# Optimization experiments

Hardware: AMD Instinct MI355X
Metric: run time of the kernel (lower is better)

The kernel has to match this reference:

```python
import jax, jax.numpy as jnp
import numpy as np

EPS = 1e-5

def _bn(x, s, b, m, v):
    # inference-mode BatchNorm2d over channel axis of NCHW
    return (x - m[None, :, None, None]) * jax.lax.rsqrt(v[None, :, None, None] + EPS) \
           * s[None, :, None, None] + b[None, :, None, None]

def _conv3(x, w):
    return jax.lax.conv_general_dilated(x, w, (1, 1), 'SAME',
                                        dimension_numbers=('NCHW', 'OIHW', 'NCHW'))

def _conv1(x, w, b):
    # 1x1 conv as einsum; w: [out_c, in_c]
    return jnp.einsum('oc,bchw->bohw', w, x) + b[None, :, None, None]

def _cca(f, qw, qb, kw, kb, vw, vb, gamma):
    # Criss-cross attention (faithful to source: no diagonal -inf masking, INF() unused there)
    B, C, H, W = f.shape
    q = _conv1(f, qw, qb)   # [B, C/8, H, W]
    k = _conv1(f, kw, kb)   # [B, C/8, H, W]
    v = _conv1(f, vw, vb)   # [B, C,   H, W]
    # energy along column (same w, all h') and row (same h, all w')
    eH = jnp.einsum('bchw,bciw->bhwi', q, k)            # [B,H,W,H]
    eW = jnp.einsum('bchw,bchj->bhwj', q, k)            # [B,H,W,W]
    att = jax.nn.softmax(jnp.concatenate([eH, eW], axis=3), axis=3)  # [B,H,W,H+W]
    aH, aW = att[..., :H], att[..., H:]
    oH = jnp.einsum('bhwi,bciw->bchw', aH, v)
    oW = jnp.einsum('bhwj,bchj->bchw', aW, v)
    return gamma * (oH + oW) + f


def setup_inputs() -> dict:
    key = jax.random.key(0)
    ks = iter(jax.random.split(key, 64))
    B, Cin, H, W = 8, 2048, 64, 64
    Ci, Cq, Co = 256, 32, 512
    rn = lambda s, sc=0.02: jax.random.normal(next(ks), s, jnp.float32) * sc
    ru = lambda s: jax.random.uniform(next(ks), s, jnp.float32)
    return {
        'x': jax.random.normal(next(ks), (B, Cin, H, W), jnp.float32),
        'recurrence': 2,
        'conva_w': rn((Ci, Cin, 3, 3)),
        'bn_a_s': ru((Ci,)), 'bn_a_b': rn((Ci,), 0.1), 'bn_a_m': rn((Ci,), 0.1), 'bn_a_v': ru((Ci,)),
        'q_w': rn((Cq, Ci)), 'q_b': rn((Cq,), 0.1),
        'k_w': rn((Cq, Ci)), 'k_b': rn((Cq,), 0.1),
        'v_w': rn((Ci, Ci)), 'v_b': rn((Ci,), 0.1),
        'cca_gamma': rn((1,), 1.0),
        'convb_w': rn((Ci, Ci, 3, 3)),
        'bn_b_s': ru((Ci,)), 'bn_b_b': rn((Ci,), 0.1), 'bn_b_m': rn((Ci,), 0.1), 'bn_b_v': ru((Ci,)),
        'sq_w': rn((Ci, Ci)), 'sq_b': rn((Ci,), 0.1),
        'bn_g_s': ru((Ci,)), 'bn_g_b': rn((Ci,), 0.1), 'bn_g_m': rn((Ci,), 0.1), 'bn_g_v': ru((Ci,)),
        'fc1_w': rn((Ci // 2, Ci)), 'fc1_b': rn((Ci // 2,), 0.1),
        'fc2_w': rn((Ci, Ci // 2)), 'fc2_b': rn((Ci,), 0.1),
        'bott_w': rn((Co, Cin + 2 * Ci, 3, 3)),
        'bn_t_s': ru((Co,)), 'bn_t_b': rn((Co,), 0.1), 'bn_t_m': rn((Co,), 0.1), 'bn_t_v': ru((Co,)),
    }


def reference(x, recurrence, conva_w, bn_a_s, bn_a_b, bn_a_m, bn_a_v,
              q_w, q_b, k_w, k_b, v_w, v_b, cca_gamma,
              convb_w, bn_b_s, bn_b_b, bn_b_m, bn_b_v,
              sq_w, sq_b, bn_g_s, bn_g_b, bn_g_m, bn_g_v,
              fc1_w, fc1_b, fc2_w, fc2_b,
              bott_w, bn_t_s, bn_t_b, bn_t_m, bn_t_v):
    out = _bn(_conv3(x, conva_w), bn_a_s, bn_a_b, bn_a_m, bn_a_v)
    # Global_Avg_Pooling (SE gating) on conva output
    fm = jax.nn.relu(_bn(_conv1(out, sq_w, sq_b), bn_g_s, bn_g_b, bn_g_m, bn_g_v))
    vec = fm.mean(axis=(-2, -1))                       # [B, Ci]
    h = jax.nn.relu(vec @ fc1_w.T + fc1_b)
    gate = jax.nn.sigmoid(h @ fc2_w.T + fc2_b)
    out_gap = out * gate[:, :, None, None]
    # recurrent criss-cross attention
    for _ in range(recurrence):
        out = _cca(out, q_w, q_b, k_w, k_b, v_w, v_b, cca_gamma)
    out = _bn(_conv3(out, convb_w), bn_b_s, bn_b_b, bn_b_m, bn_b_v)
    cat = jnp.concatenate([x, out, out_gap], axis=1)   # [B, Cin+2*Ci, H, W]
    return _bn(_conv3(cat, bott_w), bn_t_s, bn_t_b, bn_t_m, bn_t_v)
```

## Files before the change

### kernel.cpp

```cpp
#include <hip/hip_runtime.h>
#include <hip/hip_bf16.h>

typedef unsigned short u16;
typedef unsigned int u32;
typedef __attribute__((ext_vector_type(8))) short short8;
typedef __attribute__((ext_vector_type(8))) unsigned short u16x8;
typedef __attribute__((ext_vector_type(4))) unsigned short u16x4;
typedef __attribute__((ext_vector_type(4))) float f32x4;

#define BN_EPS 1e-5f
#define PADW 66
#define CATC 2560

__device__ __forceinline__ u16 f2b(float f) {
    __hip_bfloat16 h = __float2bfloat16(f);
    return *reinterpret_cast<u16*>(&h);
}
__device__ __forceinline__ float b2f(u16 u) {
    __hip_bfloat16 h;
    *reinterpret_cast<u16*>(&h) = u;
    return __bfloat162float(h);
}
__device__ __forceinline__ void async_copy16(void* lds, const void* g) {
    __builtin_amdgcn_global_load_lds((const __attribute__((address_space(1))) u32*)g,
                                     (__attribute__((address_space(3))) u32*)lds, 16, 0, 0);
}
__device__ __forceinline__ void fence_() { asm volatile("" ::: "memory"); }
__device__ __forceinline__ void barrier_() { fence_(); __builtin_amdgcn_s_barrier(); fence_(); }

template<int TAPS, int BN, int EPI, int CPT, int NTILES, int KSPLIT>
__global__ __launch_bounds__(512, 2)
void gemm8(const u16* __restrict__ Ag, int cstride,
           const u16* __restrict__ Bg, int ktot_full, int klen,
           const float* __restrict__ alpha, const float* __restrict__ beta,
           u16* __restrict__ outb, int ostride, int ochoff,
           float* __restrict__ outf, int nch)
{
    constexpr int WN   = BN / 4;
    constexpr int NSUB = WN / 16;
    constexpr int NQ   = NSUB / 2;
    constexpr int BLH  = BN / 128;
    constexpr int ASZ  = 256 * 128;
    constexpr int BSZ  = BN * 128;
    const int KT = klen / 64;

    extern __shared__ __align__(16) char smem[];
    char* smA = smem;
    char* smB = smem + 2 * ASZ;

    const int tid  = threadIdx.x;
    const int lane = tid & 63;
    const int wave = tid >> 6;
    const int wr = wave >> 2;
    const int wc = wave & 3;

    const int nwg = gridDim.x;
    const int wg  = blockIdx.x;
    const int swz = (wg & 7) * (nwg >> 3) + (wg >> 3);
    const int sel = swz % (NTILES * KSPLIT);
    const int m0  = (swz / (NTILES * KSPLIT)) * 256;
    const int n0  = (sel / KSPLIT) * BN;
    const int ks  = sel % KSPLIT;
    const int kstart = ks * klen;

    const int sr = tid >> 3;
    const int sc = tid & 7;
    const int scx8 = (sc ^ (sr & 7)) * 8;
    long baseAe[4];
#pragma unroll
    for (int j = 0; j < 4; ++j) {
        int p = m0 + j * 64 + sr;
        int b = p >> 12, h = (p >> 6) & 63, w = p & 63;
        long apix = (TAPS == 1) ? ((long)(b * PADW + h + 1) * PADW + (w + 1))
                                : ((long)(b * PADW + h) * PADW + w);
        baseAe[j] = apix * cstride + scx8;
    }
    long baseBe[2 * BLH];
#pragma unroll
    for (int h = 0; h < 2; ++h)
#pragma unroll
        for (int l = 0; l < BLH; ++l)
            baseBe[h * BLH + l] = (long)(n0 + h * (BN / 2) + l * 64 + sr) * ktot_full + scx8;

    auto stA = [&](int bsel, int h, long aoff) {
#pragma unroll
        for (int l = 0; l < 2; ++l) {
            const u16* g = Ag + baseAe[2 * h + l] + aoff;
            async_copy16(smA + bsel * ASZ + h * 16384 + l * 8192 + tid * 16, g);
        }
    };
    auto stB = [&](int bsel, int h, int k0) {
#pragma unroll
        for (int l = 0; l < BLH; ++l) {
            const u16* g = Bg + baseBe[h * BLH + l] + k0;
            async_copy16(smB + bsel * BSZ + h * (BSZ / 2) + l * 8192 + tid * 16, g);
        }
    };

    const int rsel  = lane & 15;
    const int cswz0 = (((lane >> 4)     ^ (lane & 7)) << 4);
    const int cswz1 = (((4 | (lane >> 4)) ^ (lane & 7)) << 4);

    f32x4 acc[8][NSUB] = {};
    short8 a0f[4][2], a1f[4][2], b0[NQ][2], b1[NQ][2];

    auto ldA = [&](int bsel, int mh, short8 (&aa)[4][2]) {
        const char* base = smA + bsel * ASZ + (wr * 128 + mh * 64 + rsel) * 128;
#pragma unroll
        for (int mi = 0; mi < 4; ++mi) {
            aa[mi][0] = *(const short8*)(base + mi * 2048 + cswz0);
            aa[mi][1] = *(const short8*)(base + mi * 2048 + cswz1);
        }
    };
    auto ldB = [&](int bsel, int nh, short8 (&bb)[NQ][2]) {
        const char* base = smB + bsel * BSZ + (wc * WN + nh * (WN / 2) + rsel) * 128;
#pragma unroll
        for (int nj = 0; nj < NQ; ++nj) {
            bb[nj][0] = *(const short8*)(base + nj * 2048 + cswz0);
            bb[nj][1] = *(const short8*)(base + nj * 2048 + cswz1);
        }
    };
    auto quad = [&](int MH, int NH, short8 (&aa)[4][2], short8 (&bb)[NQ][2]) {
#pragma unroll
        for (int mi = 0; mi < 4; ++mi)
#pragma unroll
            for (int nj = 0; nj < NQ; ++nj)
#pragma unroll
                for (int kk = 0; kk < 2; ++kk)
                    acc[MH * 4 + mi][NH * NQ + nj] =
                        __builtin_amdgcn_mfma_f32_16x16x32_bf16(
                            aa[mi][kk], bb[nj][kk], acc[MH * 4 + mi][NH * NQ + nj], 0, 0, 0);
    };

    const int tap0 = kstart / CPT;
    int c0_ = kstart - tap0 * CPT;
    int dx_ = tap0 % 3;
    long aoff_ = ((long)dx_ + (long)(tap0 / 3) * PADW) * cstride + c0_;
    auto adv = [&]() {
        c0_ += 64; aoff_ += 64;
        if (c0_ == CPT) {
            c0_ = 0; aoff_ += (long)cstride - CPT;
            if (++dx_ == 3) { dx_ = 0; aoff_ += (long)(PADW - 3) * cstride; }
        }
    };

    stA(0, 0, aoff_); stA(0, 1, aoff_); stB(0, 0, kstart); stB(0, 1, kstart);
    adv();
    stA(1, 0, aoff_); stA(1, 1, aoff_); stB(1, 0, kstart + 64); stB(1, 1, kstart + 64);
    int skb = kstart + 128;

    asm volatile("s_waitcnt vmcnt(8)" ::: "memory");
    barrier_();

    for (int kt = 0; kt < KT; ++kt) {
        const int buf = kt & 1;
        ldA(buf, 0, a0f); ldB(buf, 0, b0); ldB(buf, 1, b1); ldA(buf, 1, a1f);
        if (kt >= 1 && kt + 1 < KT) { stA(buf ^ 1, 0, aoff_); stA(buf ^ 1, 1, aoff_); }
        __builtin_amdgcn_s_setprio(1);
        quad(0, 0, a0f, b0);
        quad(0, 1, a0f, b1);
        __builtin_amdgcn_s_setprio(0);
        barrier_();
        if (kt + 2 < KT) { stB(buf, 0, skb); stB(buf, 1, skb); }
        __builtin_amdgcn_s_setprio(1);
        quad(1, 0, a1f, b0);
        quad(1, 1, a1f, b1);
        __builtin_amdgcn_s_setprio(0);
        if (kt + 2 < KT) {
            asm volatile("s_waitcnt vmcnt(4)" ::: "memory");
        } else {
            asm volatile("s_waitcnt vmcnt(0)" ::: "memory");
        }
        barrier_();
        adv(); skb += 64;
    }

    const int nl = lane & 15, mq = lane >> 4;
#pragma unroll
    for (int s = 0; s < 8; ++s) {
#pragma unroll
        for (int nj = 0; nj < NSUB; ++nj) {
            int n = n0 + wc * WN + nj * 16 + nl;
            float al = (EPI == 4) ? 1.f : alpha[n];
            float be = (EPI == 4) ? 0.f : beta[n];
#pragma unroll
            for (int r = 0; r < 4; ++r) {
                int m = m0 + wr * 128 + s * 16 + mq * 4 + r;
                float v = acc[s][nj][r] * al + be;
                if (EPI == 0) {
                    int b = m >> 12, h = (m >> 6) & 63, w = m & 63;
                    long addr = ((long)(b * PADW + h + 1) * PADW + (w + 1)) * ostride + ochoff + n;
                    outb[addr] = f2b(v);
                } else if (EPI == 2) {
                    int b = m >> 12, h = (m >> 6) & 63, w = m & 63;
                    outf[((long)(b * nch + n) << 12) + (h * 64 + w)] = v;
                } else {
                    outf[(long)ks * ((long)32768 * nch) + (long)m * nch + n] = v;
                }
            }
        }
    }
}

__global__ void combine_k(const float* __restrict__ P,
                          const float* __restrict__ alpha, const float* __restrict__ beta,
                          u16* __restrict__ dst, int dstride, int choff)
{
    int t = threadIdx.x;
    int m = blockIdx.x * 4 + (t >> 6);
    int n = (t & 63) * 4;
    int b = m >> 12, h = (m >> 6) & 63, w = m & 63;
    f32x4 v0 = *(const f32x4*)&P[(long)m * 256 + n];
    f32x4 v1 = *(const f32x4*)&P[(long)32768 * 256 + (long)m * 256 + n];
    f32x4 al = *(const f32x4*)&alpha[n];
    f32x4 be = *(const f32x4*)&beta[n];
    u16x4 r;
#pragma unroll
    for (int i = 0; i < 4; ++i) r[i] = f2b((v0[i] + v1[i]) * al[i] + be[i]);
    *(u16x4*)&dst[((long)(b * PADW + h + 1) * PADW + (w + 1)) * dstride + choff + n] = r;
}

__global__ void border_k(u16* __restrict__ cat, u16* __restrict__ f0)
{
    int i = blockIdx.x;
    int b = i / 260, r = i - b * 260;
    int ph, pw;
    if (r < 66)       { ph = 0;        pw = r; }
    else if (r < 132) { ph = 65;       pw = r - 66; }
    else if (r < 196) { ph = r - 131;  pw = 0; }
    else              { ph = r - 195;  pw = 65; }
    long pix = (long)(b * PADW + ph) * PADW + pw;
    int t = threadIdx.x;
    u16x8 z = {};
    *(u16x8*)&cat[pix * CATC + t * 8] = z;
    if (t < 64) *(u16x8*)&cat[pix * CATC + 2048 + t * 8] = z;
    if (t < 32) *(u16x8*)&f0[pix * 256 + t * 8] = z;
}

template<int TAPS, int EPI>
__global__ __launch_bounds__(256, 2)
void gemm_conv(const u16* __restrict__ A, int cstride, int cpt,
               const u16* __restrict__ Bw, int ktot,
               const float* __restrict__ alpha, const float* __restrict__ beta,
               u16* __restrict__ outb, int ostride, int ochoff,
               float* __restrict__ outf, int n_total)
{
    __shared__ u16 As[128][32];
    __shared__ u16 Bs[128][32];
    __shared__ float red[128];

    const int tid  = threadIdx.x;
    const int lane = tid & 63;
    const int wave = tid >> 6;
    const int wr = wave >> 1, wc = wave & 1;
    const int m0 = blockIdx.y * 128;
    const int n0 = blockIdx.x * 128;

    long pixbase[2];
    long browk[2];
#pragma unroll
    for (int i = 0; i < 2; ++i) {
        int row = i * 64 + (tid >> 2);
        int p = m0 + row;
        int b = p >> 12, h = (p >> 6) & 63, w = p & 63;
        if (TAPS == 1) pixbase[i] = (long)(b * PADW + h + 1) * PADW + (w + 1);
        else           pixbase[i] = (long)(b * PADW + h) * PADW + w;
        browk[i] = (long)(n0 + row) * ktot;
    }
    const int chunk = (tid & 3) * 8;

    f32x4 acc[4][4] = {};

    const int steps = ktot / 32;
    int c0 = 0, dx = 0;
    long toff = 0;
    for (int s = 0; s < steps; ++s) {
        const int k0 = s * 32;
#pragma unroll
        for (int i = 0; i < 2; ++i) {
            const u16* ga = A + (pixbase[i] + ((TAPS == 1) ? 0 : toff)) * cstride + c0 + chunk;
            async_copy16((char*)(&As[0][0]) + i * 4096 + tid * 16, ga);
            const u16* gb = Bw + browk[i] + k0 + chunk;
            async_copy16((char*)(&Bs[0][0]) + i * 4096 + tid * 16, gb);
        }
        asm volatile("s_waitcnt vmcnt(0)" ::: "memory");
        __syncthreads();

        short8 af[4], bf[4];
#pragma unroll
        for (int x = 0; x < 4; ++x) {
            af[x] = *(const short8*)&As[wr * 64 + x * 16 + (lane & 15)][(lane >> 4) * 8];
            bf[x] = *(const short8*)&Bs[wc * 64 + x * 16 + (lane & 15)][(lane >> 4) * 8];
        }
#pragma unroll
        for (int mi = 0; mi < 4; ++mi)
#pragma unroll
            for (int ni = 0; ni < 4; ++ni)
                acc[mi][ni] = __builtin_amdgcn_mfma_f32_16x16x32_bf16(af[mi], bf[ni], acc[mi][ni], 0, 0, 0);
        __syncthreads();

        c0 += 32;
        if (TAPS > 1 && c0 == cpt) {
            c0 = 0; dx++; toff += 1;
            if (dx == 3) { dx = 0; toff += PADW - 3; }
        }
    }

    const int nl = lane & 15;
    const int mq = lane >> 4;

    if (EPI == 3) {
        if (tid < 128) red[tid] = 0.f;
        __syncthreads();
#pragma unroll
        for (int ni = 0; ni < 4; ++ni) {
            int ncol = wc * 64 + ni * 16 + nl;
            int n = n0 + ncol;
            float aa = alpha[n], bb = beta[n];
            float ssum = 0.f;
#pragma unroll
            for (int mi = 0; mi < 4; ++mi)
#pragma unroll
                for (int r = 0; r < 4; ++r)
                    ssum += fmaxf(acc[mi][ni][r] * aa + bb, 0.f);
            atomicAdd(&red[ncol], ssum);
        }
        __syncthreads();
        if (tid < 128) {
            int b = m0 >> 12;
            atomicAdd(&outf[b * 256 + n0 + tid], red[tid]);
        }
    } else {
#pragma unroll
        for (int mi = 0; mi < 4; ++mi) {
#pragma unroll
            for (int r = 0; r < 4; ++r) {
                int m = m0 + wr * 64 + mi * 16 + mq * 4 + r;
#pragma unroll
                for (int ni = 0; ni < 4; ++ni) {
                    int n = n0 + wc * 64 + ni * 16 + nl;
                    float v = acc[mi][ni][r] * alpha[n] + beta[n];
                    outb[(long)m * ostride + n] = f2b(v);
                }
            }
        }
    }
}

__global__ void xpad_k(const float* __restrict__ x, u16* __restrict__ cat)
{
    __shared__ float T[64][68];
    int bh = blockIdx.y;
    int b = bh >> 6, h = bh & 63;
    int c0 = blockIdx.x * 64;
    int t = threadIdx.x;
    const float* xb = x + (((long)b * 2048 + c0) * 64 + h) * 64;
#pragma unroll
    for (int i = 0; i < 4; ++i) {
        int idx = i * 256 + t;
        int c = idx >> 4, wq = (idx & 15) * 4;
        *(f32x4*)&T[c][wq] = *(const f32x4*)&xb[(long)c * 4096 + wq];
    }
    __syncthreads();
    long pbase = ((long)(b * PADW + h + 1) * PADW + 1) * CATC + c0;
#pragma unroll
    for (int j = 0; j < 2; ++j) {
        int idx = j * 256 + t;
        int w = idx >> 3, cg = (idx & 7) * 8;
        u16x8 r;
#pragma unroll
        for (int u = 0; u < 8; ++u) r[u] = f2b(T[cg + u][w]);
        *(u16x8*)&cat[pbase + (long)w * CATC + cg] = r;
    }
}

__global__ void prep_w3(const float* __restrict__ w, u16* __restrict__ o, int O, int C)
{
    int idx = blockIdx.x * 256 + threadIdx.x;
    if (idx >= O * C) return;
    int oo = idx / C, c = idx - oo * C;
    const float* s = w + (long)idx * 9;
    long base = (long)oo * 9 * C + c;
#pragma unroll
    for (int t = 0; t < 9; ++t) o[base + (long)t * C] = f2b(s[t]);
}

__global__ void prep_qkv(const float* __restrict__ qw, const float* __restrict__ kw,
                         const float* __restrict__ vw, u16* __restrict__ o)
{
    int idx = blockIdx.x * 256 + threadIdx.x;
    int n = idx >> 8, c = idx & 255;
    float v;
    if (n < 32) v = qw[n * 256 + c];
    else if (n < 64) v = kw[(n - 32) * 256 + c];
    else if (n < 320) v = vw[(n - 64) * 256 + c];
    else v = 0.f;
    o[idx] = f2b(v);
}

__global__ void prep_cast(const float* __restrict__ w, u16* __restrict__ o, int n)
{
    int i = blockIdx.x * 256 + threadIdx.x;
    if (i < n) o[i] = f2b(w[i]);
}

__global__ void prep_ab(const float* as, const float* ab, const float* am, const float* av,
                        const float* gs, const float* gb, const float* gm, const float* gv, const float* sqb,
                        const float* bs, const float* bb, const float* bm, const float* bv,
                        const float* ts, const float* tb, const float* tm, const float* tv,
                        const float* qb, const float* kb, const float* vb,
                        float* Aa, float* Ba_, float* Ag, float* Bg, float* Ab2, float* Bb2,
                        float* At, float* Bt, float* Aq, float* Bq)
{
    int i = blockIdx.x * 256 + threadIdx.x;
    if (i < 256) { float al = as[i] * rsqrtf(av[i] + BN_EPS); Aa[i] = al; Ba_[i] = ab[i] - am[i] * al; }
    else if (i < 512) { int n = i - 256; float al = gs[n] * rsqrtf(gv[n] + BN_EPS); Ag[n] = al; Bg[n] = gb[n] - gm[n] * al + sqb[n] * al; }
    else if (i < 768) { int n = i - 512; float al = bs[n] * rsqrtf(bv[n] + BN_EPS); Ab2[n] = al; Bb2[n] = bb[n] - bm[n] * al; }
    else if (i < 1280) { int n = i - 768; float al = ts[n] * rsqrtf(tv[n] + BN_EPS); At[n] = al; Bt[n] = tb[n] - tm[n] * al; }
    else if (i < 1664) { int n = i - 1280; Aq[n] = 1.f; Bq[n] = (n < 32) ? qb[n] : (n < 64) ? kb[n - 32] : (n < 320) ? vb[n - 64] : 0.f; }
}

__global__ void gate_k(const float* __restrict__ vacc, const float* __restrict__ fc1w,
                       const float* __restrict__ fc1b, const float* __restrict__ fc2w,
                       const float* __restrict__ fc2b, float* __restrict__ gate)
{
    __shared__ float v[256], hbuf[128];
    int b = blockIdx.x, t = threadIdx.x;
    v[t] = vacc[b * 256 + t] * (1.f / 4096.f);
    __syncthreads();
    if (t < 128) {
        float s = fc1b[t];
        for (int c = 0; c < 256; ++c) s += v[c] * fc1w[t * 256 + c];
        hbuf[t] = fmaxf(s, 0.f);
    }
    __syncthreads();
    float s = fc2b[t];
    for (int j = 0; j < 128; ++j) s += hbuf[j] * fc2w[t * 128 + j];
    gate[b * 256 + t] = 1.f / (1.f + __expf(-s));
}

__global__ void gap_k(const u16* __restrict__ f0, const float* __restrict__ gate, u16* __restrict__ cat)
{
    int p = blockIdx.x, t = threadIdx.x;
    int b = p >> 12, h = (p >> 6) & 63, w = p & 63;
    long ppad = (long)(b * PADW + h + 1) * PADW + (w + 1);
    float f = b2f(f0[ppad * 256 + t]);
    cat[ppad * CATC + 2304 + t] = f2b(f * gate[b * 256 + t]);
}

__global__ void gram_k(const u16* __restrict__ qkv, float* eH, float* eW)
{
    __shared__ u16 Qs[64][32];
    __shared__ u16 Ks[64][32];
    int g = blockIdx.x;
    int mode = g >> 9;
    int bx = g & 511;
    int b = bx >> 6, s = bx & 63;
    float* e = mode ? eW : eH;
    int tid = threadIdx.x, lane = tid & 63, wave = tid >> 6;
    {
        int r = tid >> 2, ch = (tid & 3) * 8;
        long pix = (mode == 0) ? ((long)(b * 64 + r) * 64 + s) : ((long)(b * 64 + s) * 64 + r);
        const u16* gp = qkv + pix * 384;
        *(u16x8*)&Qs[r][ch] = *(const u16x8*)(gp + ch);
        *(u16x8*)&Ks[r][ch] = *(const u16x8*)(gp + 32 + ch);
    }
    __syncthreads();
    f32x4 acc[4] = {};
    short8 a = *(const short8*)&Qs[wave * 16 + (lane & 15)][(lane >> 4) * 8];
#pragma unroll
    for (int ni = 0; ni < 4; ++ni) {
        short8 bb = *(const short8*)&Ks[ni * 16 + (lane & 15)][(lane >> 4) * 8];
        acc[ni] = __builtin_amdgcn_mfma_f32_16x16x32_bf16(a, bb, acc[ni], 0, 0, 0);
    }
#pragma unroll
    for (int ni = 0; ni < 4; ++ni)
#pragma unroll
        for (int r = 0; r < 4; ++r) {
            int row = wave * 16 + (lane >> 4) * 4 + r;
            int col = ni * 16 + (lane & 15);
            long pix = (mode == 0) ? ((long)(b * 64 + row) * 64 + s) : ((long)(b * 64 + s) * 64 + row);
            e[pix * 64 + col] = acc[ni][r];
        }
}

__global__ void softmax_k(const float* __restrict__ eH, const float* __restrict__ eW,
                          u16* __restrict__ aH, u16* __restrict__ aW)
{
    long row = blockIdx.x * 4 + (threadIdx.x >> 6);
    int lane = threadIdx.x & 63;
    float v0 = eH[row * 64 + lane];
    float v1 = eW[row * 64 + lane];
    float m = fmaxf(v0, v1);
#pragma unroll
    for (int off = 32; off; off >>= 1) m = fmaxf(m, __shfl_xor(m, off));
    float e0 = __expf(v0 - m), e1 = __expf(v1 - m);
    float s = e0 + e1;
#pragma unroll
    for (int off = 32; off; off >>= 1) s += __shfl_xor(s, off);
    float inv = 1.f / s;
    aH[row * 64 + lane] = f2b(e0 * inv);
    aW[row * 64 + lane] = f2b(e1 * inv);
}

__global__ __launch_bounds__(256, 2)
void oh_k(const u16* __restrict__ aH, const u16* __restrict__ qkv, float* __restrict__ oHb)
{
    __shared__ float Al[64][68];
    __shared__ u16 Vl[64][264];
    int bx = blockIdx.x;
    int b = bx >> 6, w = bx & 63;
    int t = threadIdx.x;
#pragma unroll
    for (int pass = 0; pass < 2; ++pass) {
        int r = pass * 32 + (t >> 3);
        int ch = (t & 7) * 8;
        u16x8 v = *(const u16x8*)(aH + ((long)(b * 64 + r) * 64 + w) * 64 + ch);
        f32x4 s0, s1;
#pragma unroll
        for (int u = 0; u < 4; ++u) { s0[u] = b2f(v[u]); s1[u] = b2f(v[4 + u]); }
        *(f32x4*)&Al[r][ch] = s0;
        *(f32x4*)&Al[r][ch + 4] = s1;
    }
#pragma unroll
    for (int pass = 0; pass < 8; ++pass) {
        int i = pass * 8 + (t >> 5);
        int ch = (t & 31) * 8;
        *(u16x8*)&Vl[i][ch] = *(const u16x8*)(qkv + ((long)(b * 64 + i) * 64 + w) * 384 + 64 + ch);
    }
    __syncthreads();
    int hb = (t >> 5) * 8, cb = (t & 31) * 8;
    float acc[8][8] = {};
    for (int i = 0; i < 64; ++i) {
        float av[8], vv[8];
        u16x8 v8 = *(const u16x8*)&Vl[i][cb];
#pragma unroll
        for (int u = 0; u < 8; ++u) av[u] = Al[hb + u][i];
#pragma unroll
        for (int u = 0; u < 8; ++u) vv[u] = b2f(v8[u]);
#pragma unroll
        for (int u = 0; u < 8; ++u)
#pragma unroll
            for (int x = 0; x < 8; ++x)
                acc[u][x] += av[u] * vv[x];
    }
#pragma unroll
    for (int u = 0; u < 8; ++u) {
        long base = ((long)(b * 64 + hb + u) * 64 + w) * 256 + cb;
        f32x4 s0, s1;
#pragma unroll
        for (int x = 0; x < 4; ++x) { s0[x] = acc[u][x]; s1[x] = acc[u][4 + x]; }
        *(f32x4*)&oHb[base] = s0;
        *(f32x4*)&oHb[base + 4] = s1;
    }
}

__global__ __launch_bounds__(256, 2)
void ow_k(const u16* __restrict__ aW, const u16* __restrict__ qkv, const float* __restrict__ oHb,
          const u16* __restrict__ fin, u16* __restrict__ fout, const float* __restrict__ gamma_p)
{
    __shared__ float Al[64][68];
    __shared__ u16 Vl[64][264];
    int bx = blockIdx.x;
    int b = bx >> 6, h = bx & 63;
    int t = threadIdx.x;
    float gamma = gamma_p[0];
#pragma unroll
    for (int pass = 0; pass < 2; ++pass) {
        int r = pass * 32 + (t >> 3);
        int ch = (t & 7) * 8;
        u16x8 v = *(const u16x8*)(aW + ((long)(b * 64 + h) * 64 + r) * 64 + ch);
        f32x4 s0, s1;
#pragma unroll
        for (int u = 0; u < 4; ++u) { s0[u] = b2f(v[u]); s1[u] = b2f(v[4 + u]); }
        *(f32x4*)&Al[r][ch] = s0;
        *(f32x4*)&Al[r][ch + 4] = s1;
    }
#pragma unroll
    for (int pass = 0; pass < 8; ++pass) {
        int j = pass * 8 + (t >> 5);
        int ch = (t & 31) * 8;
        *(u16x8*)&Vl[j][ch] = *(const u16x8*)(qkv + ((long)(b * 64 + h) * 64 + j) * 384 + 64 + ch);
    }
    __syncthreads();
    int wb = (t >> 5) * 8, cb = (t & 31) * 8;
    float acc[8][8] = {};
    for (int j = 0; j < 64; ++j) {
        float av[8], vv[8];
        u16x8 v8 = *(const u16x8*)&Vl[j][cb];
#pragma unroll
        for (int u = 0; u < 8; ++u) av[u] = Al[wb + u][j];
#pragma unroll
        for (int u = 0; u < 8; ++u) vv[u] = b2f(v8[u]);
#pragma unroll
        for (int u = 0; u < 8; ++u)
#pragma unroll
            for (int x = 0; x < 8; ++x)
                acc[u][x] += av[u] * vv[x];
    }
#pragma unroll
    for (int u = 0; u < 8; ++u) {
        int w = wb + u;
        long pix = ((long)(b * 64 + h) * 64 + w) * 256 + cb;
        long pp = ((long)(b * PADW + h + 1) * PADW + (w + 1)) * 256 + cb;
        u16x8 f8 = *(const u16x8*)&fin[pp];
        f32x4 o0 = *(const f32x4*)&oHb[pix];
        f32x4 o1 = *(const f32x4*)&oHb[pix + 4];
        u16x8 r8;
#pragma unroll
        for (int x = 0; x < 8; ++x) {
            float o = acc[u][x] + ((x < 4) ? o0[x] : o1[x - 4]);
            r8[x] = f2b(gamma * o + b2f(f8[x]));
        }
        *(u16x8*)&fout[pp] = r8;
    }
}

extern "C" void kernel_launch(void* const* d_in, const int* in_sizes, int n_in,
                              void* d_out, int out_size, void* d_ws, size_t ws_size,
                              hipStream_t stream)
{
    const float* x       = (const float*)d_in[0];
    const float* conva_w = (const float*)d_in[2];
    const float* bn_a_s  = (const float*)d_in[3];
    const float* bn_a_b  = (const float*)d_in[4];
    const float* bn_a_m  = (const float*)d_in[5];
    const float* bn_a_v  = (const float*)d_in[6];
    const float* q_w     = (const float*)d_in[7];
    const float* q_b     = (const float*)d_in[8];
    const float* k_w     = (const float*)d_in[9];
    const float* k_b     = (const float*)d_in[10];
    const float* v_w     = (const float*)d_in[11];
    const float* v_b     = (const float*)d_in[12];
    const float* gamma   = (const float*)d_in[13];
    const float* convb_w = (const float*)d_in[14];
    const float* bn_b_s  = (const float*)d_in[15];
    const float* bn_b_b  = (const float*)d_in[16];
    const float* bn_b_m  = (const float*)d_in[17];
    const float* bn_b_v  = (const float*)d_in[18];
    const float* sq_w    = (const float*)d_in[19];
    const float* sq_b    = (const float*)d_in[20];
    const float* bn_g_s  = (const float*)d_in[21];
    const float* bn_g_b  = (const float*)d_in[22];
    const float* bn_g_m  = (const float*)d_in[23];
    const float* bn_g_v  = (const float*)d_in[24];
    const float* fc1_w   = (const float*)d_in[25];
    const float* fc1_b   = (const float*)d_in[26];
    const float* fc2_w   = (const float*)d_in[27];
    const float* fc2_b   = (const float*)d_in[28];
    const float* bott_w  = (const float*)d_in[29];
    const float* bn_t_s  = (const float*)d_in[30];
    const float* bn_t_b  = (const float*)d_in[31];
    const float* bn_t_m  = (const float*)d_in[32];
    const float* bn_t_v  = (const float*)d_in[33];

    char* ws = (char*)d_ws;
    size_t off = 0;
    auto alloc = [&](size_t bytes) { char* p = ws + off; off += (bytes + 255) & ~(size_t)255; return p; };

    u16*   CAT  = (u16*)  alloc((size_t)8 * PADW * PADW * CATC * 2);
    u16*   F0   = (u16*)  alloc((size_t)8 * PADW * PADW * 256 * 2);
    u16*   F1   = (u16*)  alloc((size_t)8 * PADW * PADW * 256 * 2);
    size_t cca_off = off;
    u16*   QKV  = (u16*)  alloc((size_t)32768 * 384 * 2);
    float* EH   = (float*)alloc((size_t)32768 * 64 * 4);
    float* EWb  = (float*)alloc((size_t)32768 * 64 * 4);
    u16*   AH   = (u16*)  alloc((size_t)32768 * 64 * 2);
    u16*   AW   = (u16*)  alloc((size_t)32768 * 64 * 2);
    float* OHB  = (float*)alloc((size_t)32768 * 256 * 4);
    float* P    = (float*)(ws + cca_off);
    u16*   WA   = (u16*)  alloc((size_t)256 * 18432 * 2);
    u16*   WB   = (u16*)  alloc((size_t)256 * 2304 * 2);
    u16*   WT   = (u16*)  alloc((size_t)512 * 23040 * 2);
    u16*   WQKV = (u16*)  alloc((size_t)384 * 256 * 2);
    u16*   WSQ  = (u16*)  alloc((size_t)256 * 256 * 2);
    float* Aa   = (float*)alloc(256 * 4);
    float* Ba_  = (float*)alloc(256 * 4);
    float* Ag   = (float*)alloc(256 * 4);
    float* Bg   = (float*)alloc(256 * 4);
    float* Ab2  = (float*)alloc(256 * 4);
    float* Bb2  = (float*)alloc(256 * 4);
    float* At   = (float*)alloc(512 * 4);
    float* Bt   = (float*)alloc(512 * 4);
    float* Aq   = (float*)alloc(384 * 4);
    float* Bq   = (float*)alloc(384 * 4);
    float* VACC = (float*)alloc(8 * 256 * 4);
    float* GATE = (float*)alloc(8 * 256 * 4);

    hipFuncSetAttribute((const void*)gemm8<9, 256, 4, 2048, 1, 2>,
                        hipFuncAttributeMaxDynamicSharedMemorySize, 131072);
    hipFuncSetAttribute((const void*)gemm8<9, 256, 4, 256, 1, 2>,
                        hipFuncAttributeMaxDynamicSharedMemorySize, 131072);
    hipFuncSetAttribute((const void*)gemm8<9, 256, 2, 2560, 2, 1>,
                        hipFuncAttributeMaxDynamicSharedMemorySize, 131072);

    hipMemsetAsync(VACC, 0, 8 * 256 * 4, stream);

    border_k<<<8 * 260, 256, 0, stream>>>(CAT, F0);
    prep_w3<<<(256 * 2048 + 255) / 256, 256, 0, stream>>>(conva_w, WA, 256, 2048);
    prep_w3<<<(256 * 256 + 255) / 256, 256, 0, stream>>>(convb_w, WB, 256, 256);
    prep_w3<<<(512 * 2560 + 255) / 256, 256, 0, stream>>>(bott_w, WT, 512, 2560);
    prep_qkv<<<384, 256, 0, stream>>>(q_w, k_w, v_w, WQKV);
    prep_cast<<<256, 256, 0, stream>>>(sq_w, WSQ, 65536);
    prep_ab<<<7, 256, 0, stream>>>(bn_a_s, bn_a_b, bn_a_m, bn_a_v,
                                   bn_g_s, bn_g_b, bn_g_m, bn_g_v, sq_b,
                                   bn_b_s, bn_b_b, bn_b_m, bn_b_v,
                                   bn_t_s, bn_t_b, bn_t_m, bn_t_v,
                                   q_b, k_b, v_b,
                                   Aa, Ba_, Ag, Bg, Ab2, Bb2, At, Bt, Aq, Bq);
    xpad_k<<<dim3(32, 512), 256, 0, stream>>>(x, CAT);

    gemm8<9, 256, 4, 2048, 1, 2><<<256, 512, 131072, stream>>>(
        CAT, CATC, WA, 18432, 9216, Aa, Ba_, nullptr, 0, 0, P, 256);
    combine_k<<<8192, 256, 0, stream>>>(P, Aa, Ba_, F0, 256, 0);

    gemm_conv<1, 3><<<dim3(2, 256), 256, 0, stream>>>(F0, 256, 256, WSQ, 256, Ag, Bg, nullptr, 0, 0, VACC, 0);
    gate_k<<<8, 256, 0, stream>>>(VACC, fc1_w, fc1_b, fc2_w, fc2_b, GATE);
    gap_k<<<32768, 256, 0, stream>>>(F0, GATE, CAT);

    for (int rec = 0; rec < 2; ++rec) {
        u16* fin = rec ? F1 : F0;
        u16* fout = rec ? F0 : F1;
        gemm_conv<1, 1><<<dim3(3, 256), 256, 0, stream>>>(fin, 256, 256, WQKV, 256, Aq, Bq, QKV, 384, 0, nullptr, 0);
        gram_k<<<1024, 256, 0, stream>>>(QKV, EH, EWb);
        softmax_k<<<8192, 256, 0, stream>>>(EH, EWb, AH, AW);
        oh_k<<<512, 256, 0, stream>>>(AH, QKV, OHB);
        ow_k<<<512, 256, 0, stream>>>(AW, QKV, OHB, fin, fout, gamma);
    }

    gemm8<9, 256, 4, 256, 1, 2><<<256, 512, 131072, stream>>>(
        F0, 256, WB, 2304, 1152, Ab2, Bb2, nullptr, 0, 0, P, 256);
    combine_k<<<8192, 256, 0, stream>>>(P, Ab2, Bb2, CAT, CATC, 2048);

    gemm8<9, 256, 2, 2560, 2, 1><<<256, 512, 131072, stream>>>(
        CAT, CATC, WT, 23040, 23040, At, Bt, nullptr, 0, 0, (float*)d_out, 512);
}
```

Baseline: 1.173 ms.

## Load GEMM weight fragments directly from global memory instead of staging in LDS

The conv-GEMM kernel stops staging the weight (B) tile through shared memory. Each wave now reads its B fragments straight from global memory into registers each k-step, and LDS use is halved to A only. The pipeline is reduced to a single barrier per iteration with a full vmcnt(0) wait. This trims LDS traffic and footprint, but the B loads become uncoalesced per-wave global reads that sit on the critical path with no prefetch. The two-phase overlap of the old loop is also lost.

```diff
diff --git a/kernel.cpp b/kernel.cpp
--- a/kernel.cpp
+++ b/kernel.cpp
@@ -39,14 +39,11 @@
     constexpr int WN   = BN / 4;
     constexpr int NSUB = WN / 16;
     constexpr int NQ   = NSUB / 2;
-    constexpr int BLH  = BN / 128;
     constexpr int ASZ  = 256 * 128;
-    constexpr int BSZ  = BN * 128;
     const int KT = klen / 64;
 
     extern __shared__ __align__(16) char smem[];
     char* smA = smem;
-    char* smB = smem + 2 * ASZ;
 
     const int tid  = threadIdx.x;
     const int lane = tid & 63;
@@ -75,12 +72,6 @@
                                 : ((long)(b * PADW + h) * PADW + w);
         baseAe[j] = apix * cstride + scx8;
     }
-    long baseBe[2 * BLH];
-#pragma unroll
-    for (int h = 0; h < 2; ++h)
-#pragma unroll
-        for (int l = 0; l < BLH; ++l)
-            baseBe[h * BLH + l] = (long)(n0 + h * (BN / 2) + l * 64 + sr) * ktot_full + scx8;
 
     auto stA = [&](int bsel, int h, long aoff) {
 #pragma unroll
@@ -89,20 +80,15 @@
             async_copy16(smA + bsel * ASZ + h * 16384 + l * 8192 + tid * 16, g);
         }
     };
-    auto stB = [&](int bsel, int h, int k0) {
-#pragma unroll
-        for (int l = 0; l < BLH; ++l) {
-            const u16* g = Bg + baseBe[h * BLH + l] + k0;
-            async_copy16(smB + bsel * BSZ + h * (BSZ / 2) + l * 8192 + tid * 16, g);
-        }
-    };
 
     const int rsel  = lane & 15;
     const int cswz0 = (((lane >> 4)     ^ (lane & 7)) << 4);
     const int cswz1 = (((4 | (lane >> 4)) ^ (lane & 7)) << 4);
 
+    const u16* Bbase = Bg + (long)(n0 + wc * 64 + rsel) * ktot_full + ((lane >> 4) * 8);
+
     f32x4 acc[8][NSUB] = {};
-    short8 a0f[4][2], a1f[4][2], b0[NQ][2], b1[NQ][2];
+    short8 a0f[4][2], a1f[4][2], bb0[NQ][2], bb1[NQ][2];
 
     auto ldA = [&](int bsel, int mh, short8 (&aa)[4][2]) {
         const char* base = smA + bsel * ASZ + (wr * 128 + mh * 64 + rsel) * 128;
@@ -112,13 +98,13 @@
             aa[mi][1] = *(const short8*)(base + mi * 2048 + cswz1);
         }
     };
-    auto ldB = [&](int bsel, int nh, short8 (&bb)[NQ][2]) {
-        const char* base = smB + bsel * BSZ + (wc * WN + nh * (WN / 2) + rsel) * 128;
-#pragma unroll
-        for (int nj = 0; nj < NQ; ++nj) {
-            bb[nj][0] = *(const short8*)(base + nj * 2048 + cswz0);
-            bb[nj][1] = *(const short8*)(base + nj * 2048 + cswz1);
-        }
+    auto ldBg = [&](int nh, int k0, short8 (&bb)[NQ][2]) {
+#pragma unroll
+        for (int nj = 0; nj < NQ; ++nj)
+#pragma unroll
+            for (int kk = 0; kk < 2; ++kk)
+                bb[nj][kk] = *(const short8*)(Bbase + (long)(nh * 32 + nj * 16) * ktot_full
+                                              + k0 + kk * 32);
     };
     auto quad = [&](int MH, int NH, short8 (&aa)[4][2], short8 (&bb)[NQ][2]) {
 #pragma unroll
@@ -144,35 +130,28 @@
         }
     };
 
-    stA(0, 0, aoff_); stA(0, 1, aoff_); stB(0, 0, kstart); stB(0, 1, kstart);
+    stA(0, 0, aoff_); stA(0, 1, aoff_);
     adv();
-    stA(1, 0, aoff_); stA(1, 1, aoff_); stB(1, 0, kstart + 64); stB(1, 1, kstart + 64);
-    int skb = kstart + 128;
-
-    asm volatile("s_waitcnt vmcnt(8)" ::: "memory");
+    stA(1, 0, aoff_); stA(1, 1, aoff_);
+
+    asm volatile("s_waitcnt vmcnt(4)" ::: "memory");
     barrier_();
 
+    int kB = kstart;
     for (int kt = 0; kt < KT; ++kt) {
         const int buf = kt & 1;
-        ldA(buf, 0, a0f); ldB(buf, 0, b0); ldB(buf, 1, b1); ldA(buf, 1, a1f);
+        ldBg(0, kB, bb0); ldBg(1, kB, bb1);
+        ldA(buf, 0, a0f); ldA(buf, 1, a1f);
         if (kt >= 1 && kt + 1 < KT) { stA(buf ^ 1, 0, aoff_); stA(buf ^ 1, 1, aoff_); }
         __builtin_amdgcn_s_setprio(1);
-        quad(0, 0, a0f, b0);
-        quad(0, 1, a0f, b1);
+        quad(0, 0, a0f, bb0);
+        quad(0, 1, a0f, bb1);
+        quad(1, 0, a1f, bb0);
+        quad(1, 1, a1f, bb1);
         __builtin_amdgcn_s_setprio(0);
+        asm volatile("s_waitcnt vmcnt(0)" ::: "memory");
         barrier_();
-        if (kt + 2 < KT) { stB(buf, 0, skb); stB(buf, 1, skb); }
-        __builtin_amdgcn_s_setprio(1);
-        quad(1, 0, a1f, b0);
-        quad(1, 1, a1f, b1);
-        __builtin_amdgcn_s_setprio(0);
-        if (kt + 2 < KT) {
-            asm volatile("s_waitcnt vmcnt(4)" ::: "memory");
-        } else {
-            asm volatile("s_waitcnt vmcnt(0)" ::: "memory");
-        }
-        barrier_();
-        adv(); skb += 64;
+        adv(); kB += 64;
     }
 
     const int nl = lane & 15, mq = lane >> 4;
@@ -688,11 +667,11 @@
     float* GATE = (float*)alloc(8 * 256 * 4);
 
     hipFuncSetAttribute((const void*)gemm8<9, 256, 4, 2048, 1, 2>,
-                        hipFuncAttributeMaxDynamicSharedMemorySize, 131072);
+                        hipFuncAttributeMaxDynamicSharedMemorySize, 65536);
     hipFuncSetAttribute((const void*)gemm8<9, 256, 4, 256, 1, 2>,
-                        hipFuncAttributeMaxDynamicSharedMemorySize, 131072);
+                        hipFuncAttributeMaxDynamicSharedMemorySize, 65536);
     hipFuncSetAttribute((const void*)gemm8<9, 256, 2, 2560, 2, 1>,
-                        hipFuncAttributeMaxDynamicSharedMemorySize, 131072);
+                        hipFuncAttributeMaxDynamicSharedMemorySize, 65536);
 
     hipMemsetAsync(VACC, 0, 8 * 256 * 4, stream);
 
@@ -710,7 +689,7 @@
                                    Aa, Ba_, Ag, Bg, Ab2, Bb2, At, Bt, Aq, Bq);
     xpad_k<<<dim3(32, 512), 256, 0, stream>>>(x, CAT);
 
-    gemm8<9, 256, 4, 2048, 1, 2><<<256, 512, 131072, stream>>>(
+    gemm8<9, 256, 4, 2048, 1, 2><<<256, 512, 65536, stream>>>(
         CAT, CATC, WA, 18432, 9216, Aa, Ba_, nullptr, 0, 0, P, 256);
     combine_k<<<8192, 256, 0, stream>>>(P, Aa, Ba_, F0, 256, 0);
 
@@ -728,10 +707,10 @@
         ow_k<<<512, 256, 0, stream>>>(AW, QKV, OHB, fin, fout, gamma);
     }
 
-    gemm8<9, 256, 4, 256, 1, 2><<<256, 512, 131072, stream>>>(
+    gemm8<9, 256, 4, 256, 1, 2><<<256, 512, 65536, stream>>>(
         F0, 256, WB, 2304, 1152, Ab2, Bb2, nullptr, 0, 0, P, 256);
     combine_k<<<8192, 256, 0, stream>>>(P, Ab2, Bb2, CAT, CATC, 2048);
 
-    gemm8<9, 256, 2, 2560, 2, 1><<<256, 512, 131072, stream>>>(
+    gemm8<9, 256, 2, 2560, 2, 1><<<256, 512, 65536, stream>>>(
         CAT, CATC, WT, 23040, 23040, At, Bt, nullptr, 0, 0, (float*)d_out, 512);
 }
```

After: 1.925 ms. +64.1%, slower.

## Restructure conv GEMM to 4 waves with 128x128 per-wave tiles

Applied to the files above, without the earlier changes.

The implicit-GEMM conv kernel goes from 512 threads (8 waves, 2x4 layout, 128x64 per wave) to 256 threads (4 waves, 2x2 layout, 128x128 per wave). The 256x256 block tile stays the same, with more async loads issued per thread and the vmcnt waits scaled to match. Each wave now reuses its LDS fragments across twice as many MFMAs, which cuts LDS read traffic per FLOP. In exchange each wave holds 256 accumulator VGPRs (64 f32x4), and there are fewer waves to hide latency.

```diff
diff --git a/kernel.cpp b/kernel.cpp
--- a/kernel.cpp
+++ b/kernel.cpp
@@ -28,20 +28,16 @@
 __device__ __forceinline__ void fence_() { asm volatile("" ::: "memory"); }
 __device__ __forceinline__ void barrier_() { fence_(); __builtin_amdgcn_s_barrier(); fence_(); }
 
-template<int TAPS, int BN, int EPI, int CPT, int NTILES, int KSPLIT>
-__global__ __launch_bounds__(512, 2)
+template<int TAPS, int EPI, int CPT, int NTILES, int KSPLIT>
+__global__ __launch_bounds__(256, 1)
 void gemm8(const u16* __restrict__ Ag, int cstride,
            const u16* __restrict__ Bg, int ktot_full, int klen,
            const float* __restrict__ alpha, const float* __restrict__ beta,
            u16* __restrict__ outb, int ostride, int ochoff,
            float* __restrict__ outf, int nch)
 {
-    constexpr int WN   = BN / 4;
-    constexpr int NSUB = WN / 16;
-    constexpr int NQ   = NSUB / 2;
-    constexpr int BLH  = BN / 128;
-    constexpr int ASZ  = 256 * 128;
-    constexpr int BSZ  = BN * 128;
+    constexpr int ASZ = 256 * 128;
+    constexpr int BSZ = 256 * 128;
     const int KT = klen / 64;
 
     extern __shared__ __align__(16) char smem[];
@@ -51,49 +47,44 @@
     const int tid  = threadIdx.x;
     const int lane = tid & 63;
     const int wave = tid >> 6;
-    const int wr = wave >> 2;
-    const int wc = wave & 3;
+    const int wr = wave >> 1;
+    const int wc = wave & 1;
 
     const int nwg = gridDim.x;
     const int wg  = blockIdx.x;
     const int swz = (wg & 7) * (nwg >> 3) + (wg >> 3);
     const int sel = swz % (NTILES * KSPLIT);
     const int m0  = (swz / (NTILES * KSPLIT)) * 256;
-    const int n0  = (sel / KSPLIT) * BN;
+    const int n0  = (sel / KSPLIT) * 256;
     const int ks  = sel % KSPLIT;
     const int kstart = ks * klen;
 
     const int sr = tid >> 3;
     const int sc = tid & 7;
     const int scx8 = (sc ^ (sr & 7)) * 8;
-    long baseAe[4];
-#pragma unroll
-    for (int j = 0; j < 4; ++j) {
-        int p = m0 + j * 64 + sr;
+    long baseAe[8];
+#pragma unroll
+    for (int j = 0; j < 8; ++j) {
+        int p = m0 + j * 32 + sr;
         int b = p >> 12, h = (p >> 6) & 63, w = p & 63;
         long apix = (TAPS == 1) ? ((long)(b * PADW + h + 1) * PADW + (w + 1))
                                 : ((long)(b * PADW + h) * PADW + w);
         baseAe[j] = apix * cstride + scx8;
     }
-    long baseBe[2 * BLH];
-#pragma unroll
-    for (int h = 0; h < 2; ++h)
-#pragma unroll
-        for (int l = 0; l < BLH; ++l)
-            baseBe[h * BLH + l] = (long)(n0 + h * (BN / 2) + l * 64 + sr) * ktot_full + scx8;
+    const long baseB0 = (long)(n0 + sr) * ktot_full + scx8;
 
     auto stA = [&](int bsel, int h, long aoff) {
 #pragma unroll
-        for (int l = 0; l < 2; ++l) {
-            const u16* g = Ag + baseAe[2 * h + l] + aoff;
-            async_copy16(smA + bsel * ASZ + h * 16384 + l * 8192 + tid * 16, g);
+        for (int l = 0; l < 4; ++l) {
+            const u16* g = Ag + baseAe[h * 4 + l] + aoff;
+            async_copy16(smA + bsel * ASZ + h * 16384 + l * 4096 + tid * 16, g);
         }
     };
     auto stB = [&](int bsel, int h, int k0) {
 #pragma unroll
-        for (int l = 0; l < BLH; ++l) {
-            const u16* g = Bg + baseBe[h * BLH + l] + k0;
-            async_copy16(smB + bsel * BSZ + h * (BSZ / 2) + l * 8192 + tid * 16, g);
+        for (int l = 0; l < 4; ++l) {
+            const u16* g = Bg + baseB0 + (long)((h * 4 + l) * 32) * ktot_full + k0;
+            async_copy16(smB + bsel * BSZ + h * 16384 + l * 4096 + tid * 16, g);
         }
     };
 
@@ -101,8 +92,8 @@
     const int cswz0 = (((lane >> 4)     ^ (lane & 7)) << 4);
     const int cswz1 = (((4 | (lane >> 4)) ^ (lane & 7)) << 4);
 
-    f32x4 acc[8][NSUB] = {};
-    short8 a0f[4][2], a1f[4][2], b0[NQ][2], b1[NQ][2];
+    f32x4 acc[8][8] = {};
+    short8 a0f[4][2], a1f[4][2], b0[4][2], b1[4][2];
 
     auto ldA = [&](int bsel, int mh, short8 (&aa)[4][2]) {
         const char* base = smA + bsel * ASZ + (wr * 128 + mh * 64 + rsel) * 128;
@@ -112,24 +103,24 @@
             aa[mi][1] = *(const short8*)(base + mi * 2048 + cswz1);
         }
     };
-    auto ldB = [&](int bsel, int nh, short8 (&bb)[NQ][2]) {
-        const char* base = smB + bsel * BSZ + (wc * WN + nh * (WN / 2) + rsel) * 128;
-#pragma unroll
-        for (int nj = 0; nj < NQ; ++nj) {
+    auto ldB = [&](int bsel, int nh, short8 (&bb)[4][2]) {
+        const char* base = smB + bsel * BSZ + (wc * 128 + nh * 64 + rsel) * 128;
+#pragma unroll
+        for (int nj = 0; nj < 4; ++nj) {
             bb[nj][0] = *(const short8*)(base + nj * 2048 + cswz0);
             bb[nj][1] = *(const short8*)(base + nj * 2048 + cswz1);
         }
     };
-    auto quad = [&](int MH, int NH, short8 (&aa)[4][2], short8 (&bb)[NQ][2]) {
+    auto quad = [&](int MH, int NH, short8 (&aa)[4][2], short8 (&bb)[4][2]) {
 #pragma unroll
         for (int mi = 0; mi < 4; ++mi)
 #pragma unroll
-            for (int nj = 0; nj < NQ; ++nj)
+            for (int nj = 0; nj < 4; ++nj)
 #pragma unroll
                 for (int kk = 0; kk < 2; ++kk)
-                    acc[MH * 4 + mi][NH * NQ + nj] =
+                    acc[MH * 4 + mi][NH * 4 + nj] =
                         __builtin_amdgcn_mfma_f32_16x16x32_bf16(
-                            aa[mi][kk], bb[nj][kk], acc[MH * 4 + mi][NH * NQ + nj], 0, 0, 0);
+                            aa[mi][kk], bb[nj][kk], acc[MH * 4 + mi][NH * 4 + nj], 0, 0, 0);
     };
 
     const int tap0 = kstart / CPT;
@@ -149,7 +140,7 @@
     stA(1, 0, aoff_); stA(1, 1, aoff_); stB(1, 0, kstart + 64); stB(1, 1, kstart + 64);
     int skb = kstart + 128;
 
-    asm volatile("s_waitcnt vmcnt(8)" ::: "memory");
+    asm volatile("s_waitcnt vmcnt(16)" ::: "memory");
     barrier_();
 
     for (int kt = 0; kt < KT; ++kt) {
@@ -167,7 +158,7 @@
         quad(1, 1, a1f, b1);
         __builtin_amdgcn_s_setprio(0);
         if (kt + 2 < KT) {
-            asm volatile("s_waitcnt vmcnt(4)" ::: "memory");
+            asm volatile("s_waitcnt vmcnt(8)" ::: "memory");
         } else {
             asm volatile("s_waitcnt vmcnt(0)" ::: "memory");
         }
@@ -179,8 +170,8 @@
 #pragma unroll
     for (int s = 0; s < 8; ++s) {
 #pragma unroll
-        for (int nj = 0; nj < NSUB; ++nj) {
-            int n = n0 + wc * WN + nj * 16 + nl;
+        for (int nj = 0; nj < 8; ++nj) {
+            int n = n0 + wc * 128 + nj * 16 + nl;
             float al = (EPI == 4) ? 1.f : alpha[n];
             float be = (EPI == 4) ? 0.f : beta[n];
 #pragma unroll
@@ -687,11 +678,11 @@
     float* VACC = (float*)alloc(8 * 256 * 4);
     float* GATE = (float*)alloc(8 * 256 * 4);
 
-    hipFuncSetAttribute((const void*)gemm8<9, 256, 4, 2048, 1, 2>,
+    hipFuncSetAttribute((const void*)gemm8<9, 4, 2048, 1, 2>,
                         hipFuncAttributeMaxDynamicSharedMemorySize, 131072);
-    hipFuncSetAttribute((const void*)gemm8<9, 256, 4, 256, 1, 2>,
+    hipFuncSetAttribute((const void*)gemm8<9, 4, 256, 1, 2>,
                         hipFuncAttributeMaxDynamicSharedMemorySize, 131072);
-    hipFuncSetAttribute((const void*)gemm8<9, 256, 2, 2560, 2, 1>,
+    hipFuncSetAttribute((const void*)gemm8<9, 2, 2560, 2, 1>,
                         hipFuncAttributeMaxDynamicSharedMemorySize, 131072);
 
     hipMemsetAsync(VACC, 0, 8 * 256 * 4, stream);
@@ -710,7 +701,7 @@
                                    Aa, Ba_, Ag, Bg, Ab2, Bb2, At, Bt, Aq, Bq);
     xpad_k<<<dim3(32, 512), 256, 0, stream>>>(x, CAT);
 
-    gemm8<9, 256, 4, 2048, 1, 2><<<256, 512, 131072, stream>>>(
+    gemm8<9, 4, 2048, 1, 2><<<256, 256, 131072, stream>>>(
         CAT, CATC, WA, 18432, 9216, Aa, Ba_, nullptr, 0, 0, P, 256);
     combine_k<<<8192, 256, 0, stream>>>(P, Aa, Ba_, F0, 256, 0);
 
@@ -728,10 +719,10 @@
         ow_k<<<512, 256, 0, stream>>>(AW, QKV, OHB, fin, fout, gamma);
     }
 
-    gemm8<9, 256, 4, 256, 1, 2><<<256, 512, 131072, stream>>>(
+    gemm8<9, 4, 256, 1, 2><<<256, 256, 131072, stream>>>(
         F0, 256, WB, 2304, 1152, Ab2, Bb2, nullptr, 0, 0, P, 256);
     combine_k<<<8192, 256, 0, stream>>>(P, Ab2, Bb2, CAT, CATC, 2048);
 
-    gemm8<9, 256, 2, 2560, 2, 1><<<256, 512, 131072, stream>>>(
+    gemm8<9, 2, 2560, 2, 1><<<256, 256, 131072, stream>>>(
         CAT, CATC, WT, 23040, 23040, At, Bt, nullptr, 0, 0, (float*)d_out, 512);
 }
```

After: 1.231 ms. 1.05x slower.
